# Optimization experiments

Hardware: AMD Instinct MI355X
Metric: run time of the kernel (lower is better)

Reference implementation:

```python
import jax, jax.numpy as jnp
import numpy as np

D = 4  # max displacement


def setup_inputs() -> dict:
    key = jax.random.key(0)
    k1, k2 = jax.random.split(key)
    feat1 = jax.random.normal(k1, (4, 64, 192, 448), dtype=jnp.float32)
    feat2 = jax.random.normal(k2, (4, 64, 192, 448), dtype=jnp.float32)
    return {"feat1": feat1, "feat2": feat2}


def reference(feat1, feat2):
    # feat1, feat2: [B, C, H, W]
    b, c, h, w = feat1.shape
    # zero-pad feat2 spatially by D on each side
    f2p = jnp.pad(feat2, ((0, 0), (0, 0), (D, D), (D, D)))
    # For each of the (2D+1)^2 displacements, channel-mean of elementwise product.
    # Loop is over a small fixed displacement set (81), not over data dims.
    cv = [
        jnp.mean(feat1 * jax.lax.dynamic_slice(f2p, (0, 0, i, j), (b, c, h, w)), axis=1)
        for i in range(2 * D + 1)
        for j in range(2 * D + 1)
    ]
    return jnp.stack(cv, axis=1)  # [B, (2D+1)^2, H, W]
```

## Files before the change

kernel.cpp:

```cpp
#include <hip/hip_runtime.h>

namespace {
constexpr int D_  = 4;
constexpr int ND  = 9;
constexpr int NK  = 81;
constexpr int B_  = 4, C_ = 64, H_ = 192, W_ = 448;

constexpr int GROUPS = 9;

constexpr int TH  = 16;
constexpr int TXN = 16;
constexpr int PX  = 2;
constexpr int TW  = TXN * PX;
constexpr int CCH = 8;
constexpr int HC  = TW + 2 * D_;
constexpr int HCP = 44;
constexpr int NTHREADS = TH * TXN;
constexpr int F4ROW = HC / 4;
constexpr int STAGE_F4 = CCH * TH * F4ROW;
constexpr int SITER = STAGE_F4 / NTHREADS;
static_assert(SITER * NTHREADS == STAGE_F4, "exact staging coverage");
}

__global__ __launch_bounds__(NTHREADS, 4)
void corr81_kernel(const float* __restrict__ f1, const float* __restrict__ f2,
                   float* __restrict__ out)
{
    __shared__ float s2[CCH * TH * HCP];

    const int tid = threadIdx.x;
    const int tx  = tid & (TXN - 1);
    const int ty  = tid >> 4;

    const int x0 = blockIdx.x * TW;
    const int y0 = blockIdx.y * TH;
    const int bz = blockIdx.z;
    const int b  = bz / GROUPS;
    const int g  = bz - b * GROUPS;

    const int gx = x0 + tx * PX;
    const int gy = y0 + ty;
    const int yb = y0 + g - D_;

    float acc[ND][PX];
#pragma unroll
    for (int j = 0; j < ND; ++j)
#pragma unroll
        for (int p = 0; p < PX; ++p) acc[j][p] = 0.f;

    const size_t plane = (size_t)H_ * W_;
    const float* f1p = f1 + (((size_t)b * C_) * H_ + gy) * W_ + gx;

    const float* sbase = s2 + ty * HCP + tx * PX;

    for (int cc = 0; cc < C_; cc += CCH) {
        __syncthreads();

#pragma unroll
        for (int i = 0; i < SITER; ++i) {
            int l   = tid + NTHREADS * i;
            int c   = l / (TH * F4ROW);
            int rem = l - c * (TH * F4ROW);
            int r   = rem / F4ROW;
            int p   = rem - r * F4ROW;
            int col = p * 4;
            int yy  = yb + r;
            int xx  = x0 - D_ + col;
            float4 v = make_float4(0.f, 0.f, 0.f, 0.f);
            if (yy >= 0 && yy < H_ && xx >= 0 && xx < W_) {
                v = *(const float4*)(f2 + (((size_t)b * C_ + cc + c) * H_ + yy) * W_ + xx);
            }
            *(float4*)&s2[(c * TH + r) * HCP + col] = v;
        }
        __syncthreads();

        float2 a[CCH];
#pragma unroll
        for (int c = 0; c < CCH; ++c)
            a[c] = *(const float2*)(f1p + (size_t)(cc + c) * plane);

#pragma unroll
        for (int c = 0; c < CCH; ++c) {
            const float* sp = sbase + c * (TH * HCP);
            float row[ND + 1];
#pragma unroll
            for (int q = 0; q < 5; ++q) {
                float2 t = *(const float2*)(sp + 2 * q);
                row[2 * q]     = t.x;
                row[2 * q + 1] = t.y;
            }
#pragma unroll
            for (int dx = 0; dx < ND; ++dx) {
                acc[dx][0] = fmaf(a[c].x, row[dx],     acc[dx][0]);
                acc[dx][1] = fmaf(a[c].y, row[dx + 1], acc[dx][1]);
            }
        }
    }

    const float scale = 1.0f / (float)C_;
    float* op = out + (((size_t)b * NK) * H_ + gy) * W_ + gx;
#pragma unroll
    for (int dx = 0; dx < ND; ++dx) {
        float2 v = make_float2(acc[dx][0] * scale, acc[dx][1] * scale);
        *(float2*)(op + (size_t)(g * ND + dx) * plane) = v;
    }
}

extern "C" void kernel_launch(void* const* d_in, const int* in_sizes, int n_in,
                              void* d_out, int out_size, void* d_ws, size_t ws_size,
                              hipStream_t stream)
{
    const float* feat1 = (const float*)d_in[0];
    const float* feat2 = (const float*)d_in[1];
    float* out = (float*)d_out;

    dim3 grid(W_ / TW, H_ / TH, B_ * GROUPS);
    dim3 block(NTHREADS);
    corr81_kernel<<<grid, block, 0, stream>>>(feat1, feat2, out);
}
```

Before: 396.6 us.

## Compute three displacement rows per block with 4-pixel threads and double-buffered staging

Each block now handles three vertical displacement rows (27 outputs per pixel) instead of one, and each thread covers four pixels. This cuts redundant re-reads of feat1 and of overlapping feat2 halo rows, and raises arithmetic per shared-memory load. The feat2 staging is double-buffered through registers so the next channel chunk's global loads overlap compute. The cost is a much larger register footprint (108 accumulators) and a lower occupancy target.

```diff
diff --git a/kernel.cpp b/kernel.cpp
--- a/kernel.cpp
+++ b/kernel.cpp
@@ -6,104 +6,142 @@
 constexpr int NK  = 81;
 constexpr int B_  = 4, C_ = 64, H_ = 192, W_ = 448;
 
-constexpr int GROUPS = 9;
+constexpr int NG  = 3;
+constexpr int GD  = 3;
 
 constexpr int TH  = 16;
 constexpr int TXN = 16;
-constexpr int PX  = 2;
+constexpr int PX  = 4;
 constexpr int TW  = TXN * PX;
-constexpr int CCH = 8;
+constexpr int CCH = 4;
+constexpr int NR  = TH + GD - 1;
 constexpr int HC  = TW + 2 * D_;
-constexpr int HCP = 44;
-constexpr int NTHREADS = TH * TXN;
-constexpr int F4ROW = HC / 4;
-constexpr int STAGE_F4 = CCH * TH * F4ROW;
-constexpr int SITER = STAGE_F4 / NTHREADS;
-static_assert(SITER * NTHREADS == STAGE_F4, "exact staging coverage");
+constexpr int HCP = 76;
+constexpr int NTH = TH * TXN;
+constexpr int F4R = HC / 4;
+constexpr int STG = CCH * NR * F4R;
+constexpr int SIT = (STG + NTH - 1) / NTH;
+constexpr int ROUNDS = C_ / CCH;
+constexpr int BUFSZ  = CCH * NR * HCP;
+constexpr int PLANE  = H_ * W_;
 }
 
-__global__ __launch_bounds__(NTHREADS, 4)
+__global__ __launch_bounds__(NTH, 2)
 void corr81_kernel(const float* __restrict__ f1, const float* __restrict__ f2,
                    float* __restrict__ out)
 {
-    __shared__ float s2[CCH * TH * HCP];
+    __shared__ float s2[2][BUFSZ];
 
     const int tid = threadIdx.x;
     const int tx  = tid & (TXN - 1);
     const int ty  = tid >> 4;
 
-    const int x0 = blockIdx.x * TW;
+    const int bx    = blockIdx.x;
+    const int tilex = bx / NG;
+    const int g     = bx - tilex * NG;
+
+    const int x0 = tilex * TW;
     const int y0 = blockIdx.y * TH;
-    const int bz = blockIdx.z;
-    const int b  = bz / GROUPS;
-    const int g  = bz - b * GROUPS;
+    const int b  = blockIdx.z;
 
     const int gx = x0 + tx * PX;
     const int gy = y0 + ty;
-    const int yb = y0 + g - D_;
+    const int yb = y0 + g * GD - D_;
 
-    float acc[ND][PX];
+    float acc[GD][ND][PX];
 #pragma unroll
-    for (int j = 0; j < ND; ++j)
+    for (int s = 0; s < GD; ++s)
 #pragma unroll
-        for (int p = 0; p < PX; ++p) acc[j][p] = 0.f;
+        for (int dx = 0; dx < ND; ++dx)
+#pragma unroll
+            for (int p = 0; p < PX; ++p) acc[s][dx][p] = 0.f;
 
-    const size_t plane = (size_t)H_ * W_;
-    const float* f1p = f1 + (((size_t)b * C_) * H_ + gy) * W_ + gx;
+    int  gidx[SIT];
+    int  lofs[SIT];
+    bool ld[SIT];
+    bool wr[SIT];
+#pragma unroll
+    for (int i = 0; i < SIT; ++i) {
+        int l   = tid + NTH * i;
+        int c   = l / (NR * F4R);
+        int rem = l - c * (NR * F4R);
+        int r   = rem / F4R;
+        int p   = rem - r * F4R;
+        int yy  = yb + r;
+        int xx  = x0 - D_ + 4 * p;
+        wr[i]   = (l < STG);
+        ld[i]   = wr[i] && (yy >= 0) && (yy < H_) && (xx >= 0) && (xx < W_);
+        int yc  = yy < 0 ? 0 : (yy >= H_ ? H_ - 1 : yy);
+        int xc  = xx < 0 ? 0 : (xx >= W_ ? W_ - 4 : xx);
+        lofs[i] = (c * NR + r) * HCP + 4 * p;
+        gidx[i] = ((b * C_ + c) * H_ + yc) * W_ + xc;
+    }
 
-    const float* sbase = s2 + ty * HCP + tx * PX;
+    float4 v[SIT];
+#pragma unroll
+    for (int i = 0; i < SIT; ++i) {
+        float4 t = make_float4(0.f, 0.f, 0.f, 0.f);
+        if (ld[i]) t = *(const float4*)(f2 + gidx[i]);
+        v[i] = t;
+    }
+#pragma unroll
+    for (int i = 0; i < SIT; ++i)
+        if (wr[i]) *(float4*)&s2[0][lofs[i]] = v[i];
 
-    for (int cc = 0; cc < C_; cc += CCH) {
+    const float* f1q = f1 + ((size_t)(b * C_) * H_ + gy) * W_ + gx;
+    float* const opb = out + ((size_t)(b * NK) * H_ + gy) * W_ + gx;
+
+#pragma unroll 2
+    for (int rr = 0; rr < ROUNDS; ++rr) {
+        const int cur = rr & 1;
         __syncthreads();
 
+        if (rr + 1 < ROUNDS) {
+            const int cof = (rr + 1) * CCH * PLANE;
 #pragma unroll
-        for (int i = 0; i < SITER; ++i) {
-            int l   = tid + NTHREADS * i;
-            int c   = l / (TH * F4ROW);
-            int rem = l - c * (TH * F4ROW);
-            int r   = rem / F4ROW;
-            int p   = rem - r * F4ROW;
-            int col = p * 4;
-            int yy  = yb + r;
-            int xx  = x0 - D_ + col;
-            float4 v = make_float4(0.f, 0.f, 0.f, 0.f);
-            if (yy >= 0 && yy < H_ && xx >= 0 && xx < W_) {
-                v = *(const float4*)(f2 + (((size_t)b * C_ + cc + c) * H_ + yy) * W_ + xx);
+            for (int i = 0; i < SIT; ++i) {
+                float4 t = make_float4(0.f, 0.f, 0.f, 0.f);
+                if (ld[i]) t = *(const float4*)(f2 + gidx[i] + cof);
+                v[i] = t;
             }
-            *(float4*)&s2[(c * TH + r) * HCP + col] = v;
         }
-        __syncthreads();
 
-        float2 a[CCH];
-#pragma unroll
-        for (int c = 0; c < CCH; ++c)
-            a[c] = *(const float2*)(f1p + (size_t)(cc + c) * plane);
-
+        const float* sb = &s2[cur][0];
 #pragma unroll
         for (int c = 0; c < CCH; ++c) {
-            const float* sp = sbase + c * (TH * HCP);
-            float row[ND + 1];
+            float4 af = *(const float4*)(f1q + (size_t)(rr * CCH + c) * PLANE);
+            float a_[PX] = {af.x, af.y, af.z, af.w};
 #pragma unroll
-            for (int q = 0; q < 5; ++q) {
-                float2 t = *(const float2*)(sp + 2 * q);
-                row[2 * q]     = t.x;
-                row[2 * q + 1] = t.y;
+            for (int s = 0; s < GD; ++s) {
+                const float* rp = sb + (c * NR + ty + s) * HCP + 4 * tx;
+                float r_[12];
+                *(float4*)&r_[0] = *(const float4*)(rp);
+                *(float4*)&r_[4] = *(const float4*)(rp + 4);
+                *(float4*)&r_[8] = *(const float4*)(rp + 8);
+#pragma unroll
+                for (int dx = 0; dx < ND; ++dx)
+#pragma unroll
+                    for (int p = 0; p < PX; ++p)
+                        acc[s][dx][p] = fmaf(a_[p], r_[p + dx], acc[s][dx][p]);
             }
+        }
+
+        if (rr + 1 < ROUNDS) {
 #pragma unroll
-            for (int dx = 0; dx < ND; ++dx) {
-                acc[dx][0] = fmaf(a[c].x, row[dx],     acc[dx][0]);
-                acc[dx][1] = fmaf(a[c].y, row[dx + 1], acc[dx][1]);
-            }
+            for (int i = 0; i < SIT; ++i)
+                if (wr[i]) *(float4*)&s2[cur ^ 1][lofs[i]] = v[i];
         }
     }
 
     const float scale = 1.0f / (float)C_;
-    float* op = out + (((size_t)b * NK) * H_ + gy) * W_ + gx;
 #pragma unroll
-    for (int dx = 0; dx < ND; ++dx) {
-        float2 v = make_float2(acc[dx][0] * scale, acc[dx][1] * scale);
-        *(float2*)(op + (size_t)(g * ND + dx) * plane) = v;
-    }
+    for (int s = 0; s < GD; ++s)
+#pragma unroll
+        for (int dx = 0; dx < ND; ++dx) {
+            float4 w4 = make_float4(acc[s][dx][0] * scale, acc[s][dx][1] * scale,
+                                    acc[s][dx][2] * scale, acc[s][dx][3] * scale);
+            *(float4*)(opb + (size_t)((g * GD + s) * ND + dx) * PLANE) = w4;
+        }
 }
 
 extern "C" void kernel_launch(void* const* d_in, const int* in_sizes, int n_in,
@@ -114,7 +152,7 @@
     const float* feat2 = (const float*)d_in[1];
     float* out = (float*)d_out;
 
-    dim3 grid(W_ / TW, H_ / TH, B_ * GROUPS);
-    dim3 block(NTHREADS);
+    dim3 grid((W_ / TW) * NG, H_ / TH, B_);
+    dim3 block(NTH);
     corr81_kernel<<<grid, block, 0, stream>>>(feat1, feat2, out);
 }
```

After: 949.2 us. 139% more time.

## Widen per-thread tile to 4 pixels and reorder grid so displacement groups share tiles

Applied to the files above, without the earlier changes.

Each thread now computes 4 horizontal pixels instead of 2, so the tile widens to 64 columns and f1 loads, LDS reads and output stores become float4. The grid puts the 9 vertical-displacement groups innermost in blockIdx.x, so blocks reading the same f1/f2 tile are scheduled close together and hit in L2. The staging loop is replaced by per-thread fixed-address float4 loads, with a small edge path for the halo, which removes the index division arithmetic. Risks are higher register pressure from 36 accumulators and fewer blocks in the grid.

```diff
diff --git a/kernel.cpp b/kernel.cpp
--- a/kernel.cpp
+++ b/kernel.cpp
@@ -6,23 +6,19 @@
 constexpr int NK  = 81;
 constexpr int B_  = 4, C_ = 64, H_ = 192, W_ = 448;
 
-constexpr int GROUPS = 9;
-
 constexpr int TH  = 16;
 constexpr int TXN = 16;
-constexpr int PX  = 2;
+constexpr int PX  = 4;
 constexpr int TW  = TXN * PX;
 constexpr int CCH = 8;
 constexpr int HC  = TW + 2 * D_;
-constexpr int HCP = 44;
-constexpr int NTHREADS = TH * TXN;
-constexpr int F4ROW = HC / 4;
-constexpr int STAGE_F4 = CCH * TH * F4ROW;
-constexpr int SITER = STAGE_F4 / NTHREADS;
-static_assert(SITER * NTHREADS == STAGE_F4, "exact staging coverage");
+constexpr int HCP = 76;
+constexpr int NTH = TH * TXN;
+constexpr int ROUNDS = C_ / CCH;
+constexpr int PLANE  = H_ * W_;
 }
 
-__global__ __launch_bounds__(NTHREADS, 4)
+__global__ __launch_bounds__(NTH, 4)
 void corr81_kernel(const float* __restrict__ f1, const float* __restrict__ f2,
                    float* __restrict__ out)
 {
@@ -32,77 +28,89 @@
     const int tx  = tid & (TXN - 1);
     const int ty  = tid >> 4;
 
-    const int x0 = blockIdx.x * TW;
+    const int bx    = blockIdx.x;
+    const int tilex = bx / ND;
+    const int g     = bx - tilex * ND;
+
+    const int x0 = tilex * TW;
     const int y0 = blockIdx.y * TH;
-    const int bz = blockIdx.z;
-    const int b  = bz / GROUPS;
-    const int g  = bz - b * GROUPS;
+    const int b  = blockIdx.z;
 
     const int gx = x0 + tx * PX;
     const int gy = y0 + ty;
-    const int yb = y0 + g - D_;
+
+    const int  yy  = y0 + g - D_ + ty;
+    const bool okY = (yy >= 0) && (yy < H_);
+    const int  yc  = yy < 0 ? 0 : (yy >= H_ ? H_ - 1 : yy);
+
+    const int  xxM = x0 - 4 + 4 * tx;
+    const bool okM = okY && (xxM >= 0);
+    const int  xcM = xxM < 0 ? 0 : xxM;
+
+    const int  xxE = x0 + 60 + 4 * tx;
+    const bool okE = okY && (xxE + 3 < W_);
+    const int  xcE = okE ? xxE : 0;
+
+    const size_t f2b = (size_t)(b * C_) * PLANE;
+    const float* f2M = f2 + f2b + (size_t)yc * W_ + xcM;
+    const float* f2E = f2 + f2b + (size_t)yc * W_ + xcE;
+
+    float* const sM = s2 + ty * HCP + 4 * tx;
+    float* const sE = s2 + ty * HCP + 64 + 4 * tx;
+    const float* const sbase = s2 + ty * HCP + 4 * tx;
+
+    const float* f1q = f1 + ((size_t)(b * C_) * H_ + gy) * W_ + gx;
 
     float acc[ND][PX];
 #pragma unroll
-    for (int j = 0; j < ND; ++j)
+    for (int dx = 0; dx < ND; ++dx)
 #pragma unroll
-        for (int p = 0; p < PX; ++p) acc[j][p] = 0.f;
+        for (int p = 0; p < PX; ++p) acc[dx][p] = 0.f;
 
-    const size_t plane = (size_t)H_ * W_;
-    const float* f1p = f1 + (((size_t)b * C_) * H_ + gy) * W_ + gx;
+    for (int rr = 0; rr < ROUNDS; ++rr) {
+        __syncthreads();
+        const size_t coff = (size_t)(rr * CCH) * PLANE;
 
-    const float* sbase = s2 + ty * HCP + tx * PX;
-
-    for (int cc = 0; cc < C_; cc += CCH) {
+#pragma unroll
+        for (int c = 0; c < CCH; ++c) {
+            float4 t = make_float4(0.f, 0.f, 0.f, 0.f);
+            if (okM) t = *(const float4*)(f2M + coff + (size_t)c * PLANE);
+            *(float4*)(sM + c * (TH * HCP)) = t;
+        }
+        if (tx < 2) {
+#pragma unroll
+            for (int c = 0; c < CCH; ++c) {
+                float4 t = make_float4(0.f, 0.f, 0.f, 0.f);
+                if (okE) t = *(const float4*)(f2E + coff + (size_t)c * PLANE);
+                *(float4*)(sE + c * (TH * HCP)) = t;
+            }
+        }
         __syncthreads();
 
 #pragma unroll
-        for (int i = 0; i < SITER; ++i) {
-            int l   = tid + NTHREADS * i;
-            int c   = l / (TH * F4ROW);
-            int rem = l - c * (TH * F4ROW);
-            int r   = rem / F4ROW;
-            int p   = rem - r * F4ROW;
-            int col = p * 4;
-            int yy  = yb + r;
-            int xx  = x0 - D_ + col;
-            float4 v = make_float4(0.f, 0.f, 0.f, 0.f);
-            if (yy >= 0 && yy < H_ && xx >= 0 && xx < W_) {
-                v = *(const float4*)(f2 + (((size_t)b * C_ + cc + c) * H_ + yy) * W_ + xx);
-            }
-            *(float4*)&s2[(c * TH + r) * HCP + col] = v;
-        }
-        __syncthreads();
-
-        float2 a[CCH];
+        for (int c = 0; c < CCH; ++c) {
+            float4 af = *(const float4*)(f1q + coff + (size_t)c * PLANE);
+            float a_[PX] = {af.x, af.y, af.z, af.w};
+            const float* rp = sbase + c * (TH * HCP);
+            float r_[12];
+            *(float4*)&r_[0] = *(const float4*)(rp);
+            *(float4*)&r_[4] = *(const float4*)(rp + 4);
+            *(float4*)&r_[8] = *(const float4*)(rp + 8);
 #pragma unroll
-        for (int c = 0; c < CCH; ++c)
-            a[c] = *(const float2*)(f1p + (size_t)(cc + c) * plane);
-
+            for (int dx = 0; dx < ND; ++dx)
 #pragma unroll
-        for (int c = 0; c < CCH; ++c) {
-            const float* sp = sbase + c * (TH * HCP);
-            float row[ND + 1];
-#pragma unroll
-            for (int q = 0; q < 5; ++q) {
-                float2 t = *(const float2*)(sp + 2 * q);
-                row[2 * q]     = t.x;
-                row[2 * q + 1] = t.y;
-            }
-#pragma unroll
-            for (int dx = 0; dx < ND; ++dx) {
-                acc[dx][0] = fmaf(a[c].x, row[dx],     acc[dx][0]);
-                acc[dx][1] = fmaf(a[c].y, row[dx + 1], acc[dx][1]);
-            }
+                for (int p = 0; p < PX; ++p)
+                    acc[dx][p] = fmaf(a_[p], r_[p + dx], acc[dx][p]);
         }
     }
 
     const float scale = 1.0f / (float)C_;
-    float* op = out + (((size_t)b * NK) * H_ + gy) * W_ + gx;
+    float* const op = out + ((size_t)(b * NK) * H_ + gy) * W_ + gx;
 #pragma unroll
     for (int dx = 0; dx < ND; ++dx) {
-        float2 v = make_float2(acc[dx][0] * scale, acc[dx][1] * scale);
-        *(float2*)(op + (size_t)(g * ND + dx) * plane) = v;
+        float4 w4 = make_float4(acc[dx][0] * scale, acc[dx][1] * scale,
+                                acc[dx][2] * scale, acc[dx][3] * scale);
+        *(float4*)(op + (size_t)(g * ND + dx) * PLANE) = w4;
     }
 }
 
@@ -114,7 +122,7 @@
     const float* feat2 = (const float*)d_in[1];
     float* out = (float*)d_out;
 
-    dim3 grid(W_ / TW, H_ / TH, B_ * GROUPS);
-    dim3 block(NTHREADS);
+    dim3 grid((W_ / TW) * ND, H_ / TH, B_);
+    dim3 block(NTH);
     corr81_kernel<<<grid, block, 0, stream>>>(feat1, feat2, out);
 }
```

New measurement: 440.5 us. 1.11x slower.
